# Performance work log

Measured on AMD Instinct MI355X. Metric: run time of the kernel, lower is better.

Reference implementation:

```python
import jax, jax.numpy as jnp
import numpy as np

H = 15  # hidden_size_
NUM_LAYERS = 4


def lstm_layer(x, Wih, Whh, bih, bhh):
    # x: [B, T, D] -> [B, T, H]; PyTorch gate order: i, f, g, o
    B = x.shape[0]
    h0 = jnp.zeros((B, H), x.dtype)
    c0 = jnp.zeros((B, H), x.dtype)
    b = (bih + bhh).astype(x.dtype)

    def step(carry, xt):
        h, c = carry
        g = xt @ Wih.T + h @ Whh.T + b  # [B, 4H]
        i, f, gg, o = jnp.split(g, 4, axis=-1)
        i = jax.nn.sigmoid(i)
        f = jax.nn.sigmoid(f)
        gg = jnp.tanh(gg)
        o = jax.nn.sigmoid(o)
        c = f * c + i * gg
        h = o * jnp.tanh(c)
        return (h, c), h

    _, ys = jax.lax.scan(step, (h0, c0), jnp.swapaxes(x, 0, 1))  # [T, B, H]
    return jnp.swapaxes(ys, 0, 1)


def setup_inputs() -> dict:
    key = jax.random.key(0)
    ks = jax.random.split(key, 8)
    B, T, D = 512, 2048, 64
    emb = jax.random.normal(ks[0], (B, T, D), dtype=jnp.float32)
    # pack_padded_sequence needs lengths sorted descending, min length 1
    lengths = jnp.sort(jax.random.randint(ks[1], (B,), 1, T + 1))[::-1]
    s = 0.1
    W_ih0 = jax.random.normal(ks[2], (4 * H, D), dtype=jnp.float32) * s
    W_ihr = jax.random.normal(ks[3], (NUM_LAYERS - 1, 4 * H, H), dtype=jnp.float32) * s
    W_hh = jax.random.normal(ks[4], (NUM_LAYERS, 4 * H, H), dtype=jnp.float32) * s
    b_ih = jax.random.normal(ks[5], (NUM_LAYERS, 4 * H), dtype=jnp.float32) * s
    b_hh = jax.random.normal(ks[6], (NUM_LAYERS, 4 * H), dtype=jnp.float32) * s
    return {"embeddings": emb, "lengths": lengths, "W_ih0": W_ih0,
            "W_ihr": W_ihr, "W_hh": W_hh, "b_ih": b_ih, "b_hh": b_hh}


def reference(embeddings, lengths, W_ih0, W_ihr, W_hh, b_ih, b_hh):
    # 4-layer LSTM (eval mode: inter-layer dropout is identity).
    # Running the full padded length is equivalent to packed processing for the
    # gathered outputs, since output at t < length depends only on steps <= t.
    x = lstm_layer(embeddings, W_ih0, W_hh[0], b_ih[0], b_hh[0])
    for l in range(NUM_LAYERS - 1):
        x = lstm_layer(x, W_ihr[l], W_hh[l + 1], b_ih[l + 1], b_hh[l + 1])
    # gather last valid timestep per sequence: out[b, lengths[b]-1, :]
    idx = jnp.broadcast_to((lengths - 1)[:, None, None], (x.shape[0], 1, x.shape[2]))
    return jnp.take_along_axis(x, idx, axis=1).squeeze(1)  # [B, H]
```

## Files before the change

### kernel.cpp

```cpp
#include <hip/hip_runtime.h>

#define HID 15
#define NG  60
#define DIM 64
#define T2  2048
#define NLAY 4
#define BSZ 512
#define DG  8
#define RS  16

__device__ __forceinline__ float bfr(float x) {
    unsigned u = __float_as_uint(x);
    u = (u + 0x7FFFu + ((u >> 16) & 1u)) & 0xFFFF0000u;
    return __uint_as_float(u);
}
#define CH(acc, a, b) acc = bfr(acc + bfr((a) * (b)))

__device__ __forceinline__ float tanh_np(float z) {
    const float e = __expf(-2.0f * z);
    return bfr((1.0f - e) / (1.0f + e));
}
__device__ __forceinline__ float sig_np(float z) {
    const float e   = bfr(__expf(-z));
    const float den = bfr(1.0f + e);
    return bfr(1.0f / den);
}
__device__ __forceinline__ float b2f(unsigned b) {
    return __uint_as_float(b << 16);
}

__global__ __launch_bounds__(256, 1)
void proj0(const float* __restrict__ emb,
           const int*   __restrict__ lengths,
           const float* __restrict__ Wih0,
           unsigned short* __restrict__ pa)
{
    const int wave = threadIdx.x >> 6;
    const int lane = threadIdx.x & 63;
    const int g    = (lane < NG) ? lane : (NG - 1);

    __shared__ __align__(16) float xrow[4][2][64];

    float wx[DIM];
    #pragma unroll
    for (int q = 0; q < 16; ++q) {
        float4 w = *(const float4*)(Wih0 + g*DIM + 4*q);
        wx[4*q+0] = bfr(w.x); wx[4*q+1] = bfr(w.y);
        wx[4*q+2] = bfr(w.z); wx[4*q+3] = bfr(w.w);
    }

    const int npairs = (BSZ * T2) / 2;
    const int stride = gridDim.x * 4;
    const int p0     = blockIdx.x * 4 + wave;

    float xr0 = 0.0f, xr1 = 0.0f;
    if (p0 < npairs) {
        xr0 = emb[(size_t)(2*p0)     * DIM + lane];
        xr1 = emb[(size_t)(2*p0 + 1) * DIM + lane];
    }

    for (int p = p0; p < npairs; p += stride) {
        const int pn = p + stride;
        float xn0 = 0.0f, xn1 = 0.0f;
        if (pn < npairs) {
            xn0 = emb[(size_t)(2*pn)     * DIM + lane];
            xn1 = emb[(size_t)(2*pn + 1) * DIM + lane];
        }

        const int r   = 2 * p;
        const int b   = r >> 11;
        const int t   = r & (T2 - 1);
        const int len = lengths[b];

        if (t < len) {
            xrow[wave][0][lane] = bfr(xr0);
            xrow[wave][1][lane] = bfr(xr1);
            const float4* xv0 = (const float4*)xrow[wave][0];
            const float4* xv1 = (const float4*)xrow[wave][1];
            float a0 = 0.0f, a1 = 0.0f;
            #pragma unroll
            for (int q = 0; q < 16; ++q) {
                float4 u = xv0[q]; float4 v = xv1[q];
                CH(a0, u.x, wx[4*q+0]); CH(a1, v.x, wx[4*q+0]);
                CH(a0, u.y, wx[4*q+1]); CH(a1, v.y, wx[4*q+1]);
                CH(a0, u.z, wx[4*q+2]); CH(a1, v.z, wx[4*q+2]);
                CH(a0, u.w, wx[4*q+3]); CH(a1, v.w, wx[4*q+3]);
            }
            if (lane < NG) {
                pa[(size_t)r * NG + g] = (unsigned short)(__float_as_uint(a0) >> 16);
                if (t + 1 < len)
                    pa[(size_t)(r + 1) * NG + g] = (unsigned short)(__float_as_uint(a1) >> 16);
            }
        }
        xr0 = xn0; xr1 = xn1;
    }
}

__global__ __launch_bounds__(256, 1)
void lstm4_pipe(const int* __restrict__ lengths,
                const unsigned short* __restrict__ pa,
                const float* __restrict__ Wihr,
                const float* __restrict__ Whh,
                const float* __restrict__ bih,
                const float* __restrict__ bhh,
                float* __restrict__ out)
{
    const int s    = blockIdx.x;
    const int wave = threadIdx.x >> 6;
    const int lane = threadIdx.x & 63;
    const int g    = (lane < NG) ? lane : (NG - 1);

    __shared__ __align__(16) float ring[NLAY-1][RS][16];

    const int l = wave;
    float wr[16], wi[16];
    #pragma unroll
    for (int j = 0; j < HID; ++j) wr[j] = bfr(Whh[(l*NG + g)*HID + j]);
    wr[15] = 0.0f;
    if (l > 0) {
        #pragma unroll
        for (int j = 0; j < HID; ++j) wi[j] = bfr(Wihr[((l-1)*NG + g)*HID + j]);
        wi[15] = 0.0f;
    } else {
        #pragma unroll
        for (int j = 0; j < 16; ++j) wi[j] = 0.0f;
    }
    const float bias_ = bfr(bfr(bih[l*NG + g]) + bfr(bhh[l*NG + g]));

    int len = lengths[s];
    len = len < 1 ? 1 : (len > T2 ? T2 : len);
    const unsigned short* pas = pa + (size_t)s * T2 * NG;

    float c_ = 0.0f;
    float hs[HID];
    #pragma unroll
    for (int j = 0; j < HID; ++j) hs[j] = 0.0f;

    unsigned pan_c[DG], pan_n[DG];
    if (l == 0) {
        #pragma unroll
        for (int d = 0; d < DG; ++d) {
            const int tt = (d < len) ? d : (len - 1);
            pan_n[d] = pas[(size_t)tt * NG + g];
        }
    }

    const bool tg = (lane >= 30 && lane < 45);
    const int ngrp = (len + DG - 1) / DG;
    const int G    = ngrp + NLAY - 1;

    for (int grp = 0; grp < G; ++grp) {
        const int myg = grp - l;
        if (myg >= 0 && myg < ngrp) {
            const int t0 = myg * DG;

            if (l == 0) {
                #pragma unroll
                for (int d = 0; d < DG; ++d) pan_c[d] = pan_n[d];
                #pragma unroll
                for (int d = 0; d < DG; ++d) {
                    int tt = t0 + DG + d; tt = (tt < len) ? tt : (len - 1);
                    pan_n[d] = pas[(size_t)tt * NG + g];
                }
            }

            #pragma unroll
            for (int d = 0; d < DG; ++d) {
                const int t = t0 + d;
                if (t < len) {
                    float a_in = 0.0f, a_rec = 0.0f;
                    float hv[16];

                    if (l > 0) {
                        const float4* hp = (const float4*)ring[l-1][t & (RS-1)];
                        *(float4*)&hv[0]  = hp[0]; *(float4*)&hv[4]  = hp[1];
                        *(float4*)&hv[8]  = hp[2]; *(float4*)&hv[12] = hp[3];
                    }

                    #pragma unroll
                    for (int j = 0; j < HID; ++j) CH(a_rec, hs[j], wr[j]);

                    if (l == 0) {
                        a_in = b2f(pan_c[d]);
                    } else {
                        #pragma unroll
                        for (int j = 0; j < HID; ++j) CH(a_in, hv[j], wi[j]);
                    }

                    const float z = bfr(bfr(a_in + a_rec) + bias_);
                    const float a = tg ? tanh_np(z) : sig_np(z);

                    const float fv = __shfl(a, (lane + 15) & 63);
                    const float gv = __shfl(a, (lane + 30) & 63);
                    const float ov = __shfl(a, (lane + 45) & 63);

                    const float cn = bfr(bfr(fv * c_) + bfr(a * gv));
                    c_ = cn;
                    const float hn = bfr(ov * tanh_np(cn));

                    #pragma unroll
                    for (int j = 0; j < HID; ++j)
                        hs[j] = __uint_as_float(__builtin_amdgcn_readlane(__float_as_uint(hn), j));

                    if (l < NLAY - 1 && lane < HID) ring[l][t & (RS-1)][lane] = hn;
                    if (l == NLAY - 1 && t == len - 1 && lane < HID)
                        out[s * HID + lane] = hn;
                }
            }
        }
        __syncthreads();
    }
}

__global__ __launch_bounds__(64, 1)
void lstm4_bf16np(const float* __restrict__ emb,
                  const int*   __restrict__ lengths,
                  const float* __restrict__ Wih0,
                  const float* __restrict__ Wihr,
                  const float* __restrict__ Whh,
                  const float* __restrict__ bih,
                  const float* __restrict__ bhh,
                  float* __restrict__ out)
{
    const int s    = blockIdx.x;
    const int lane = threadIdx.x;
    const int g    = (lane < NG) ? lane : (NG - 1);

    __shared__ __align__(16) float x_lds[DIM];
    __shared__ __align__(16) float h_lds[NLAY][16];

    float wx[DIM];
    #pragma unroll
    for (int q = 0; q < DIM/4; ++q) {
        float4 w = *(const float4*)(Wih0 + g*DIM + 4*q);
        wx[4*q+0] = bfr(w.x); wx[4*q+1] = bfr(w.y);
        wx[4*q+2] = bfr(w.z); wx[4*q+3] = bfr(w.w);
    }
    float wr[NLAY][16]; float wi[NLAY-1][16]; float bias[NLAY];
    #pragma unroll
    for (int l = 0; l < NLAY; ++l) {
        #pragma unroll
        for (int j = 0; j < HID; ++j) wr[l][j] = bfr(Whh[(l*NG + g)*HID + j]);
        wr[l][15] = 0.0f;
        bias[l] = bfr(bfr(bih[l*NG + g]) + bfr(bhh[l*NG + g]));
    }
    #pragma unroll
    for (int l = 0; l < NLAY-1; ++l) {
        #pragma unroll
        for (int j = 0; j < HID; ++j) wi[l][j] = bfr(Wihr[(l*NG + g)*HID + j]);
        wi[l][15] = 0.0f;
    }
    if (lane < 16) {
        #pragma unroll
        for (int l = 0; l < NLAY; ++l) h_lds[l][lane] = 0.0f;
    }
    float c[NLAY] = {0.0f, 0.0f, 0.0f, 0.0f};
    int len = lengths[s];
    len = len < 1 ? 1 : (len > T2 ? T2 : len);
    const float* xb = emb + (size_t)s * T2 * DIM;
    x_lds[lane] = bfr(xb[lane]);
    __syncthreads();
    const bool tg = (lane >= 30 && lane < 45);
    const float4* x4 = (const float4*)x_lds;
    float hout = 0.0f;
    for (int t = 0; t < len; ++t) {
        const int tn = (t + 1 < len) ? (t + 1) : t;
        const float xn = bfr(xb[(size_t)tn * DIM + lane]);
        #pragma unroll
        for (int l = 0; l < NLAY; ++l) {
            float a_in = 0.0f;
            if (l == 0) {
                #pragma unroll
                for (int q = 0; q < 16; ++q) {
                    float4 v = x4[q];
                    CH(a_in, v.x, wx[4*q+0]); CH(a_in, v.y, wx[4*q+1]);
                    CH(a_in, v.z, wx[4*q+2]); CH(a_in, v.w, wx[4*q+3]);
                }
            } else {
                const float4* hp = (const float4*)h_lds[l-1];
                float hv[16];
                *(float4*)&hv[0]  = hp[0]; *(float4*)&hv[4]  = hp[1];
                *(float4*)&hv[8]  = hp[2]; *(float4*)&hv[12] = hp[3];
                #pragma unroll
                for (int j = 0; j < HID; ++j) CH(a_in, hv[j], wi[l-1][j]);
            }
            float a_rec = 0.0f;
            {
                const float4* hc = (const float4*)h_lds[l];
                float hv[16];
                *(float4*)&hv[0]  = hc[0]; *(float4*)&hv[4]  = hc[1];
                *(float4*)&hv[8]  = hc[2]; *(float4*)&hv[12] = hc[3];
                #pragma unroll
                for (int j = 0; j < HID; ++j) CH(a_rec, hv[j], wr[l][j]);
            }
            const float z = bfr(bfr(a_in + a_rec) + bias[l]);
            const float a = tg ? tanh_np(z) : sig_np(z);
            const float fv = __shfl(a, (lane + 15) & 63);
            const float gv = __shfl(a, (lane + 30) & 63);
            const float ov = __shfl(a, (lane + 45) & 63);
            const float cn = bfr(bfr(fv * c[l]) + bfr(a * gv));
            c[l] = cn;
            const float hn = bfr(ov * tanh_np(cn));
            if (lane < HID) h_lds[l][lane] = hn;
            if (l == NLAY-1 && t == len-1) hout = hn;
        }
        x_lds[lane] = xn;
    }
    if (lane < HID) out[s * HID + lane] = hout;
}

extern "C" void kernel_launch(void* const* d_in, const int* in_sizes, int n_in,
                              void* d_out, int out_size, void* d_ws, size_t ws_size,
                              hipStream_t stream) {
    const float* emb     = (const float*)d_in[0];
    const int*   lengths = (const int*)  d_in[1];
    const float* Wih0    = (const float*)d_in[2];
    const float* Wihr    = (const float*)d_in[3];
    const float* Whh     = (const float*)d_in[4];
    const float* bih     = (const float*)d_in[5];
    const float* bhh     = (const float*)d_in[6];
    float* out = (float*)d_out;

    const size_t need = (size_t)BSZ * T2 * NG * sizeof(unsigned short);
    if (ws_size >= need) {
        unsigned short* pa = (unsigned short*)d_ws;
        proj0<<<2048, 256, 0, stream>>>(emb, lengths, Wih0, pa);
        lstm4_pipe<<<BSZ, 256, 0, stream>>>(lengths, pa, Wihr, Whh, bih, bhh, out);
    } else {
        lstm4_bf16np<<<BSZ, 64, 0, stream>>>(emb, lengths, Wih0, Wihr, Whh, bih, bhh, out);
    }
}
```

Measured before the change: 2.367 ms.

## Interleave LSTM gate lanes for DPP quad broadcast and prefetch next input projection

Gate rows are remapped so the four gates of each hidden unit sit in adjacent lanes of a quad. Gate values can then be exchanged with DPP quad_perm moves instead of ds_bpermute-based __shfl. The input projection for step t+1 is computed during step t, moving that dot product off the serial dependency chain. The sigmoid and tanh evaluation is merged into a single exp per lane. The ring buffer is zero-initialised and a barrier is added before the loop, and the readlane indices now use stride 4.

```diff
diff --git a/kernel.cpp b/kernel.cpp
--- a/kernel.cpp
+++ b/kernel.cpp
@@ -28,6 +28,8 @@
 __device__ __forceinline__ float b2f(unsigned b) {
     return __uint_as_float(b << 16);
 }
+#define QB(x, CTRL) __uint_as_float((unsigned)__builtin_amdgcn_mov_dpp( \
+        (int)__float_as_uint(x), (CTRL), 0xF, 0xF, false))
 
 __global__ __launch_bounds__(256, 1)
 void proj0(const float* __restrict__ emb,
@@ -108,24 +110,28 @@
     const int s    = blockIdx.x;
     const int wave = threadIdx.x >> 6;
     const int lane = threadIdx.x & 63;
-    const int g    = (lane < NG) ? lane : (NG - 1);
+    const int k    = lane & 3;
+    const int jq   = lane >> 2;
+    const int j_c  = (jq < HID) ? jq : (HID - 1);
+    const int row  = k * HID + j_c;
 
     __shared__ __align__(16) float ring[NLAY-1][RS][16];
 
+    for (int i = threadIdx.x; i < (NLAY-1)*RS*16; i += 256)
+        ((float*)ring)[i] = 0.0f;
+
     const int l = wave;
-    float wr[16], wi[16];
-    #pragma unroll
-    for (int j = 0; j < HID; ++j) wr[j] = bfr(Whh[(l*NG + g)*HID + j]);
-    wr[15] = 0.0f;
+    float wr[HID], wi[HID];
+    #pragma unroll
+    for (int h = 0; h < HID; ++h) wr[h] = bfr(Whh[(l*NG + row)*HID + h]);
     if (l > 0) {
         #pragma unroll
-        for (int j = 0; j < HID; ++j) wi[j] = bfr(Wihr[((l-1)*NG + g)*HID + j]);
-        wi[15] = 0.0f;
+        for (int h = 0; h < HID; ++h) wi[h] = bfr(Wihr[((l-1)*NG + row)*HID + h]);
     } else {
         #pragma unroll
-        for (int j = 0; j < 16; ++j) wi[j] = 0.0f;
-    }
-    const float bias_ = bfr(bfr(bih[l*NG + g]) + bfr(bhh[l*NG + g]));
+        for (int h = 0; h < HID; ++h) wi[h] = 0.0f;
+    }
+    const float bias_ = bfr(bfr(bih[l*NG + row]) + bfr(bhh[l*NG + row]));
 
     int len = lengths[s];
     len = len < 1 ? 1 : (len > T2 ? T2 : len);
@@ -134,20 +140,22 @@
     float c_ = 0.0f;
     float hs[HID];
     #pragma unroll
-    for (int j = 0; j < HID; ++j) hs[j] = 0.0f;
+    for (int h = 0; h < HID; ++h) hs[h] = 0.0f;
 
     unsigned pan_c[DG], pan_n[DG];
     if (l == 0) {
         #pragma unroll
         for (int d = 0; d < DG; ++d) {
             const int tt = (d < len) ? d : (len - 1);
-            pan_n[d] = pas[(size_t)tt * NG + g];
-        }
-    }
-
-    const bool tg = (lane >= 30 && lane < 45);
+            pan_n[d] = pas[(size_t)tt * NG + row];
+        }
+    }
+
+    const bool tg  = (k == 2);
     const int ngrp = (len + DG - 1) / DG;
     const int G    = ngrp + NLAY - 1;
+
+    __syncthreads();
 
     for (int grp = 0; grp < G; ++grp) {
         const int myg = grp - l;
@@ -160,51 +168,77 @@
                 #pragma unroll
                 for (int d = 0; d < DG; ++d) {
                     int tt = t0 + DG + d; tt = (tt < len) ? tt : (len - 1);
-                    pan_n[d] = pas[(size_t)tt * NG + g];
+                    pan_n[d] = pas[(size_t)tt * NG + row];
                 }
+            }
+
+            float ain_cur = 0.0f;
+            if (l == 0) {
+                ain_cur = b2f(pan_c[0]);
+            } else {
+                float hv[16];
+                const float4* hp = (const float4*)ring[l-1][t0 & (RS-1)];
+                *(float4*)&hv[0] = hp[0]; *(float4*)&hv[4]  = hp[1];
+                *(float4*)&hv[8] = hp[2]; *(float4*)&hv[12] = hp[3];
+                #pragma unroll
+                for (int h = 0; h < HID; ++h) CH(ain_cur, hv[h], wi[h]);
             }
 
             #pragma unroll
             for (int d = 0; d < DG; ++d) {
                 const int t = t0 + d;
                 if (t < len) {
-                    float a_in = 0.0f, a_rec = 0.0f;
-                    float hv[16];
-
+                    float ain_next = 0.0f;
+                    float hvn[16];
+                    const bool nx = (d < DG-1) && (t + 1 < len);
+                    if (l > 0 && nx) {
+                        const float4* hp = (const float4*)ring[l-1][(t+1) & (RS-1)];
+                        *(float4*)&hvn[0] = hp[0]; *(float4*)&hvn[4]  = hp[1];
+                        *(float4*)&hvn[8] = hp[2]; *(float4*)&hvn[12] = hp[3];
+                    }
+
+                    float a_rec = 0.0f;
+                    #pragma unroll
+                    for (int h = 0; h < HID; ++h) CH(a_rec, hs[h], wr[h]);
                     if (l > 0) {
-                        const float4* hp = (const float4*)ring[l-1][t & (RS-1)];
-                        *(float4*)&hv[0]  = hp[0]; *(float4*)&hv[4]  = hp[1];
-                        *(float4*)&hv[8]  = hp[2]; *(float4*)&hv[12] = hp[3];
+                        if (nx) {
+                            #pragma unroll
+                            for (int h = 0; h < HID; ++h) CH(ain_next, hvn[h], wi[h]);
+                        }
+                    } else {
+                        if (d < DG-1) ain_next = b2f(pan_c[d+1]);
                     }
 
-                    #pragma unroll
-                    for (int j = 0; j < HID; ++j) CH(a_rec, hs[j], wr[j]);
-
-                    if (l == 0) {
-                        a_in = b2f(pan_c[d]);
-                    } else {
-                        #pragma unroll
-                        for (int j = 0; j < HID; ++j) CH(a_in, hv[j], wi[j]);
-                    }
-
-                    const float z = bfr(bfr(a_in + a_rec) + bias_);
-                    const float a = tg ? tanh_np(z) : sig_np(z);
-
-                    const float fv = __shfl(a, (lane + 15) & 63);
-                    const float gv = __shfl(a, (lane + 30) & 63);
-                    const float ov = __shfl(a, (lane + 45) & 63);
-
-                    const float cn = bfr(bfr(fv * c_) + bfr(a * gv));
+                    const float z = bfr(bfr(ain_cur + a_rec) + bias_);
+
+                    const float arg = tg ? (-2.0f * z) : (-z);
+                    const float e   = __expf(arg);
+                    const float ea  = bfr(e);
+                    const float dns = bfr(1.0f + ea);
+                    const float rs_ = bfr(1.0f / dns);
+                    const float rt_ = bfr((1.0f - e) / (1.0f + e));
+                    const float a   = tg ? rt_ : rs_;
+
+                    const float iv = QB(a, 0x00);
+                    const float fv = QB(a, 0x55);
+                    const float gv = QB(a, 0xAA);
+                    const float ov = QB(a, 0xFF);
+
+                    const float cn = bfr(bfr(fv * c_) + bfr(iv * gv));
                     c_ = cn;
                     const float hn = bfr(ov * tanh_np(cn));
 
                     #pragma unroll
-                    for (int j = 0; j < HID; ++j)
-                        hs[j] = __uint_as_float(__builtin_amdgcn_readlane(__float_as_uint(hn), j));
-
-                    if (l < NLAY - 1 && lane < HID) ring[l][t & (RS-1)][lane] = hn;
-                    if (l == NLAY - 1 && t == len - 1 && lane < HID)
-                        out[s * HID + lane] = hn;
+                    for (int h = 0; h < HID; ++h)
+                        hs[h] = __uint_as_float(
+                            __builtin_amdgcn_readlane(__float_as_uint(hn), 4*h));
+
+                    if (l < NLAY-1 && lane < NG && k == 0)
+                        ring[l][t & (RS-1)][jq] = hn;
+                    if (l == NLAY-1 && t == len-1 && lane < NG && k == 0)
+                        out[s * HID + jq] = hn;
+
+                    ain_cur = ain_next;
                 }
             }
         }
```

Measured after the change: 2.473 ms. +4.5%, slower.
